# Performance work log

Measured on AMD Instinct MI355X. Metric: run time of the kernel, lower is better.

The kernel has to match this reference:

```python
import jax, jax.numpy as jnp
import numpy as np

N = 100000
E = 6400000
H = 64  # hidden_nf


def setup_inputs() -> dict:
    key = jax.random.key(0)
    ks = jax.random.split(key, 12)
    x = jax.random.normal(ks[0], (N, 3), dtype=jnp.float32)
    vel = jax.random.normal(ks[1], (N, 3), dtype=jnp.float32)
    vel_norm = jax.random.uniform(ks[2], (N, 1), dtype=jnp.float32)
    edge_index = jax.random.randint(ks[3], (2, E), 0, N, dtype=jnp.int32)
    # coord_mlp_vel: Linear(1,H) -> LeakyReLU(0.2) -> Linear(H,1)
    W1 = jax.random.normal(ks[4], (H, 1), dtype=jnp.float32) * (1.0 / np.sqrt(1))
    b1 = jnp.zeros((H,), dtype=jnp.float32)
    W2 = jax.random.normal(ks[5], (1, H), dtype=jnp.float32) * (1.0 / np.sqrt(H))
    b2 = jnp.zeros((1,), dtype=jnp.float32)
    # phi: Linear(1,H) -> LeakyReLU(0.2) -> Linear(H,1,bias=False, xavier gain=0.001) -> Tanh
    Wp1 = jax.random.normal(ks[6], (H, 1), dtype=jnp.float32) * (1.0 / np.sqrt(1))
    bp1 = jnp.zeros((H,), dtype=jnp.float32)
    Wp2 = jax.random.normal(ks[7], (1, H), dtype=jnp.float32) * 0.001
    return {"x": x, "vel_norm": vel_norm, "vel": vel, "edge_index": edge_index,
            "W1": W1, "b1": b1, "W2": W2, "b2": b2,
            "Wp1": Wp1, "bp1": bp1, "Wp2": Wp2}


def reference(x, vel_norm, vel, edge_index, W1, b1, W2, b2, Wp1, bp1, Wp2):
    row, col = edge_index[0], edge_index[1]
    # edge_model: gather endpoint positions, radial distance -> tiny MLP -> scaled diff
    x_diff = x[row] - x[col]                                   # [E, 3]
    radial = jnp.sqrt(jnp.sum(x_diff * x_diff, axis=1, keepdims=True))  # [E, 1]
    h = jax.nn.leaky_relu(radial @ Wp1.T + bp1, 0.2)           # [E, H]
    e_out = jnp.tanh(h @ Wp2.T)                                # [E, 1]
    m_ij = x_diff * e_out                                      # [E, 3]
    # node_model: unsorted_segment_mean over row
    agg_sum = jax.ops.segment_sum(m_ij, row, num_segments=x.shape[0])           # [N, 3]
    cnt = jax.ops.segment_sum(jnp.ones((m_ij.shape[0], 1), m_ij.dtype), row,
                              num_segments=x.shape[0])                           # [N, 1]
    x_out = x + agg_sum / jnp.maximum(cnt, 1.0)
    # velocity term: x + vel * coord_mlp_vel(vel_norm)
    hv = jax.nn.leaky_relu(vel_norm @ W1.T + b1, 0.2)          # [N, H]
    scale = hv @ W2.T + b2                                     # [N, 1]
    return x_out + vel * scale
```

## Files before the change

kernel.cpp:

```cpp
#include <hip/hip_runtime.h>
#include <hip/hip_fp16.h>
#include <math.h>

#define LEAKY 0.2f
#define HDIM 64
#define EPB 2048
#define TPB1 256
#define PERT (EPB / TPB1)
#define RANGE 1024
#define RSH 10
#define KMAX 128
#define NSUB 4
#define NSLICE 8
#define FS2 262144.0f
#define INVFS2 (1.0f / 262144.0f)
#define FBIAS 4194304


__device__ __forceinline__ float fast_tanh(float v) {
    float e = __builtin_amdgcn_exp2f(v * 2.88539008178f);
    return 1.0f - 2.0f * __builtin_amdgcn_rcpf(e + 1.0f);
}

__device__ __forceinline__ float edge_eo(float rad, float C, bool slow,
                                         const float* sW1, const float* sb1,
                                         const float* sW2) {
    if (!slow) return fast_tanh(C * rad);
    float a = 0.f;
    #pragma unroll
    for (int k = 0; k < HDIM; k++) {
        float h = fmaf(rad, sW1[k], sb1[k]);
        h = (h > 0.f) ? h : LEAKY * h;
        a = fmaf(sW2[k], h, a);
    }
    return fast_tanh(a);
}

__global__ void repack_h_kernel(const float* __restrict__ x, uint2* __restrict__ xh, int N,
                                const float* __restrict__ Wp1, const float* __restrict__ bp1,
                                const float* __restrict__ Wp2, float* __restrict__ consts,
                                uint4* __restrict__ acc4, unsigned* __restrict__ cursor, int K) {
    int i = blockIdx.x * blockDim.x + threadIdx.x;
    if (i < N) {
        unsigned hx = __half_as_ushort(__float2half(x[3*i]));
        unsigned hy = __half_as_ushort(__float2half(x[3*i+1]));
        unsigned hz = __half_as_ushort(__float2half(x[3*i+2]));
        xh[i] = make_uint2((hy << 16) | hx, hz);
        acc4[i] = make_uint4(0u, 0u, 0u, 0u);
    }
    if (blockIdx.x == 0) {
        if (threadIdx.x < 64) {
            int k = threadIdx.x;
            float w1 = Wp1[k];
            float slope = (w1 >= 0.f) ? 1.f : LEAKY;
            float c = Wp2[k] * w1 * slope;
            float bnz = (bp1[k] != 0.f) ? 1.f : 0.f;
            #pragma unroll
            for (int off = 32; off > 0; off >>= 1) {
                c += __shfl_down(c, off, 64);
                bnz += __shfl_down(bnz, off, 64);
            }
            if (k == 0) { consts[0] = c; consts[1] = bnz; }
        }
        for (int k = threadIdx.x; k < NSUB * K; k += 256) cursor[k] = 0u;
    }
}

__device__ __forceinline__ unsigned long long pack_rec(float dx, float dy, float dz,
                                                       float eo, unsigned lid) {
    unsigned hx = __half_as_ushort(__float2half(dx * eo));
    unsigned hy = __half_as_ushort(__float2half(dy * eo));
    unsigned hz = __half_as_ushort(__float2half(dz * eo));
    return (unsigned long long)lid
         | ((unsigned long long)hx << 11)
         | ((unsigned long long)hy << 27)
         | ((unsigned long long)hz << 43);
}

__device__ __forceinline__ uint2 make_record(uint2 ga, uint2 gb, int r,
                                             float C, bool slow,
                                             const float* sW1, const float* sb1,
                                             const float* sW2) {
    float ax = __half2float(__ushort_as_half((unsigned short)(ga.x & 0xFFFF)));
    float ay = __half2float(__ushort_as_half((unsigned short)(ga.x >> 16)));
    float az = __half2float(__ushort_as_half((unsigned short)(ga.y & 0xFFFF)));
    float bx = __half2float(__ushort_as_half((unsigned short)(gb.x & 0xFFFF)));
    float by = __half2float(__ushort_as_half((unsigned short)(gb.x >> 16)));
    float bz = __half2float(__ushort_as_half((unsigned short)(gb.y & 0xFFFF)));
    float dx = ax - bx, dy = ay - by, dz = az - bz;
    float rad = sqrtf(dx*dx + dy*dy + dz*dz);
    float eo = edge_eo(rad, C, slow, sW1, sb1, sW2);
    unsigned long long u = pack_rec(dx, dy, dz, eo, (unsigned)r & (RANGE - 1));
    return make_uint2((unsigned)u, (unsigned)(u >> 32));
}

__device__ __forceinline__ void rec_to_acc4(uint2 r, unsigned b_, unsigned* acc4) {
    unsigned long long u = ((unsigned long long)r.y << 32) | r.x;
    unsigned lid = (unsigned)(u & (RANGE - 1));
    unsigned node = b_ * RANGE + lid;
    float mx = __half2float(__ushort_as_half((unsigned short)((u >> 11) & 0xFFFF)));
    float my = __half2float(__ushort_as_half((unsigned short)((u >> 27) & 0xFFFF)));
    float mz = __half2float(__ushort_as_half((unsigned short)((u >> 43) & 0xFFFF)));
    atomicAdd(&acc4[4*node + 0], (unsigned)__float2int_rn(mx * FS2));
    atomicAdd(&acc4[4*node + 1], (unsigned)__float2int_rn(my * FS2));
    atomicAdd(&acc4[4*node + 2], (unsigned)__float2int_rn(mz * FS2));
    atomicAdd(&acc4[4*node + 3], 1u);
}

__global__ __launch_bounds__(TPB1) void fused4_kernel(
        const uint2* __restrict__ xh,
        const int* __restrict__ ei,
        const float* __restrict__ Wp1, const float* __restrict__ bp1,
        const float* __restrict__ Wp2, const float* __restrict__ consts,
        unsigned* __restrict__ cursor, unsigned* __restrict__ acc4,
        uint2* __restrict__ recs, int E, int K, unsigned csub) {
    __shared__ uint2 stage[EPB];
    __shared__ unsigned char bucket_of[EPB];
    __shared__ unsigned hist[KMAX];
    __shared__ unsigned scanv[KMAX + 1];
    __shared__ unsigned gstart[KMAX];
    __shared__ float sW1[HDIM], sb1[HDIM], sW2[HDIM];
    const float C = consts[0];
    const bool slow = (consts[1] != 0.f);
    const unsigned sub = (unsigned)blockIdx.x & (NSUB - 1);
    if (slow) {
        for (int k = threadIdx.x; k < HDIM; k += TPB1) {
            sW1[k] = Wp1[k]; sb1[k] = bp1[k]; sW2[k] = Wp2[k];
        }
    }
    for (int k = threadIdx.x; k < K; k += TPB1) hist[k] = 0;
    __syncthreads();

    const size_t base = (size_t)blockIdx.x * EPB;
    const unsigned t = threadIdx.x;
    uint2 rc[PERT];
    unsigned bk[PERT];
    if (base + EPB <= (size_t)E && (E & 3) == 0) {
        const int4* pr = (const int4*)(ei + base);
        const int4* pc = (const int4*)(ei + (size_t)E + base);
        int4 rv0 = pr[t];
        int4 rv1 = pr[t + TPB1];
        int4 cv0 = pc[t];
        int4 cv1 = pc[t + TPB1];
        uint2 ga0 = xh[rv0.x], ga1 = xh[rv0.y], ga2 = xh[rv0.z], ga3 = xh[rv0.w];
        uint2 ga4 = xh[rv1.x], ga5 = xh[rv1.y], ga6 = xh[rv1.z], ga7 = xh[rv1.w];
        uint2 gb0 = xh[cv0.x], gb1 = xh[cv0.y], gb2 = xh[cv0.z], gb3 = xh[cv0.w];
        uint2 gb4 = xh[cv1.x], gb5 = xh[cv1.y], gb6 = xh[cv1.z], gb7 = xh[cv1.w];
        rc[0] = make_record(ga0, gb0, rv0.x, C, slow, sW1, sb1, sW2);
        rc[1] = make_record(ga1, gb1, rv0.y, C, slow, sW1, sb1, sW2);
        rc[2] = make_record(ga2, gb2, rv0.z, C, slow, sW1, sb1, sW2);
        rc[3] = make_record(ga3, gb3, rv0.w, C, slow, sW1, sb1, sW2);
        rc[4] = make_record(ga4, gb4, rv1.x, C, slow, sW1, sb1, sW2);
        rc[5] = make_record(ga5, gb5, rv1.y, C, slow, sW1, sb1, sW2);
        rc[6] = make_record(ga6, gb6, rv1.z, C, slow, sW1, sb1, sW2);
        rc[7] = make_record(ga7, gb7, rv1.w, C, slow, sW1, sb1, sW2);
        bk[0] = (unsigned)rv0.x >> RSH; bk[1] = (unsigned)rv0.y >> RSH;
        bk[2] = (unsigned)rv0.z >> RSH; bk[3] = (unsigned)rv0.w >> RSH;
        bk[4] = (unsigned)rv1.x >> RSH; bk[5] = (unsigned)rv1.y >> RSH;
        bk[6] = (unsigned)rv1.z >> RSH; bk[7] = (unsigned)rv1.w >> RSH;
        #pragma unroll
        for (int i = 0; i < PERT; i++) atomicAdd(&hist[bk[i]], 1u);
    } else {
        #pragma unroll
        for (int i = 0; i < PERT; i++) {
            size_t e = base + (size_t)i * TPB1 + t;
            bk[i] = 0xFFFFFFFFu;
            if (e < (size_t)E) {
                int r = ei[e];
                int c = ei[(size_t)E + e];
                uint2 ga = xh[r], gb = xh[c];
                rc[i] = make_record(ga, gb, r, C, slow, sW1, sb1, sW2);
                bk[i] = (unsigned)r >> RSH;
                atomicAdd(&hist[bk[i]], 1u);
            }
        }
    }
    __syncthreads();
    unsigned res = 0, myc = 0;
    if (t < (unsigned)K) {
        myc = hist[t];
        if (myc) res = atomicAdd(&cursor[t * NSUB + sub], myc);
    }
    if (t >= 192) {
        int l = t - 192;
        unsigned origA = (l < K) ? hist[l] : 0u;
        unsigned origB = (l + 64 < K) ? hist[l + 64] : 0u;
        unsigned a = origA, b = origB;
        #pragma unroll
        for (int off = 1; off < 64; off <<= 1) {
            unsigned va = __shfl_up(a, off, 64);
            unsigned vb = __shfl_up(b, off, 64);
            if (l >= off) { a += va; b += vb; }
        }
        unsigned totA = __shfl(a, 63, 64);
        unsigned grand = totA + __shfl(b, 63, 64);
        scanv[l] = a - origA;
        scanv[l + 64] = totA + b - origB;
        if (l == 63) scanv[K] = grand;
    }
    __syncthreads();
    if (t < (unsigned)K) gstart[t] = res;
    for (int k = t; k < K; k += TPB1) hist[k] = scanv[k];
    __syncthreads();
    #pragma unroll
    for (int i = 0; i < PERT; i++) {
        if (bk[i] != 0xFFFFFFFFu) {
            unsigned slot = atomicAdd(&hist[bk[i]], 1u);
            stage[slot] = rc[i];
            bucket_of[slot] = (unsigned char)bk[i];
        }
    }
    __syncthreads();
    unsigned total = scanv[K];
    for (unsigned j = t; j < total; j += TPB1) {
        unsigned b_ = bucket_of[j];
        unsigned off = gstart[b_] + (j - scanv[b_]);
        if (off < csub) recs[(size_t)(b_ * NSUB + sub) * csub + off] = stage[j];
        else            rec_to_acc4(stage[j], b_, acc4);
    }
}

__device__ __forceinline__ void proc_rec2(uint2 rv,
                                          unsigned long long* accA,
                                          unsigned long long* accB) {
    unsigned long long u = ((unsigned long long)rv.y << 32) | rv.x;
    unsigned lid = (unsigned)(u & (RANGE - 1));
    float mx = __half2float(__ushort_as_half((unsigned short)((u >> 11) & 0xFFFF)));
    float my = __half2float(__ushort_as_half((unsigned short)((u >> 27) & 0xFFFF)));
    float mz = __half2float(__ushort_as_half((unsigned short)((u >> 43) & 0xFFFF)));
    unsigned ix = (unsigned)(__float2int_rn(mx * FS2) + FBIAS);
    unsigned iy = (unsigned)(__float2int_rn(my * FS2) + FBIAS);
    unsigned iz = (unsigned)(__float2int_rn(mz * FS2) + FBIAS);
    atomicAdd(&accA[lid], ((unsigned long long)ix << 32) | (unsigned long long)iy);
    atomicAdd(&accB[lid], ((unsigned long long)iz << 32) | 1ull);
}

__global__ __launch_bounds__(256) void reduce4_kernel(
        const uint2* __restrict__ recs, const unsigned* __restrict__ cursor,
        uint4* __restrict__ slices, int N, int K, unsigned csub) {
    __shared__ unsigned long long accA[RANGE];
    __shared__ unsigned long long accB[RANGE];
    const int b = blockIdx.x / NSLICE;
    const int s = blockIdx.x % NSLICE;
    const int r = s & (NSUB - 1);
    const int p = s / NSUB;
    for (int i = threadIdx.x; i < RANGE; i += 256) { accA[i] = 0ull; accB[i] = 0ull; }
    __syncthreads();
    unsigned cnt = cursor[b * NSUB + r];
    if (cnt > csub) cnt = csub;
    unsigned per = (cnt + 1) >> 1;
    unsigned st = (unsigned)p * per;
    unsigned en = st + per; if (en > cnt) en = cnt;
    const uint2* rb = recs + (size_t)(b * NSUB + r) * csub;
    unsigned j = st + threadIdx.x;
    if (st < cnt) {
        while (j + 256 < en) {
            uint2 r0 = rb[j];
            uint2 r1 = rb[j + 256];
            proc_rec2(r0, accA, accB);
            proc_rec2(r1, accA, accB);
            j += 512;
        }
        while (j < en) { proc_rec2(rb[j], accA, accB); j += 256; }
    }
    __syncthreads();
    const int nbase = b * RANGE;
    for (int i = threadIdx.x; i < RANGE; i += 256) {
        int node = nbase + i;
        if (node < N) {
            unsigned long long A = accA[i], B = accB[i];
            slices[(size_t)s * N + node] =
                make_uint4((unsigned)(A >> 32), (unsigned)A,
                           (unsigned)(B >> 32), (unsigned)B);
        }
    }
}

__global__ void node_merge_kernel(const float* __restrict__ x,
                                  const float* __restrict__ vel_norm,
                                  const float* __restrict__ vel,
                                  const float* __restrict__ W1, const float* __restrict__ b1,
                                  const float* __restrict__ W2, const float* __restrict__ b2,
                                  const uint4* __restrict__ slices,
                                  const uint4* __restrict__ acc4,
                                  float* __restrict__ out, int N) {
    __shared__ float sW1[HDIM], sb1[HDIM], sW2[HDIM];
    for (int k = threadIdx.x; k < HDIM; k += blockDim.x) {
        sW1[k] = W1[k]; sb1[k] = b1[k]; sW2[k] = W2[k];
    }
    __syncthreads();
    int i = blockIdx.x * blockDim.x + threadIdx.x;
    if (i >= N) return;
    unsigned long long sxb = 0, syb = 0, szb = 0;
    unsigned sc = 0;
    #pragma unroll
    for (int s = 0; s < NSLICE; s++) {
        uint4 v = slices[(size_t)s * N + i];
        sxb += v.x; syb += v.y; szb += v.z; sc += v.w;
    }
    uint4 a4 = acc4[i];
    long long fx = (long long)sxb - (long long)sc * (long long)FBIAS + (long long)(int)a4.x;
    long long fy = (long long)syb - (long long)sc * (long long)FBIAS + (long long)(int)a4.y;
    long long fz = (long long)szb - (long long)sc * (long long)FBIAS + (long long)(int)a4.z;
    float cntf = (float)(sc + a4.w);
    float sx = (float)fx * INVFS2;
    float sy = (float)fy * INVFS2;
    float sz = (float)fz * INVFS2;
    float vn = vel_norm[i];
    float a = b2[0];
    #pragma unroll
    for (int k = 0; k < HDIM; k++) {
        float h = fmaf(vn, sW1[k], sb1[k]);
        h = (h > 0.f) ? h : LEAKY * h;
        a = fmaf(sW2[k], h, a);
    }
    float inv = 1.0f / fmaxf(cntf, 1.0f);
    out[3*i]     = x[3*i]     + sx * inv + vel[3*i]     * a;
    out[3*i + 1] = x[3*i + 1] + sy * inv + vel[3*i + 1] * a;
    out[3*i + 2] = x[3*i + 2] + sz * inv + vel[3*i + 2] * a;
}

__global__ void precompute_kernel(const float* __restrict__ Wp1,
                                  const float* __restrict__ bp1,
                                  const float* __restrict__ Wp2,
                                  float* __restrict__ consts) {
    int k = threadIdx.x;
    float w1 = Wp1[k];
    float slope = (w1 >= 0.f) ? 1.f : LEAKY;
    float c = Wp2[k] * w1 * slope;
    float bnz = (bp1[k] != 0.f) ? 1.f : 0.f;
    #pragma unroll
    for (int off = 32; off > 0; off >>= 1) {
        c += __shfl_down(c, off, 64);
        bnz += __shfl_down(bnz, off, 64);
    }
    if (k == 0) { consts[0] = c; consts[1] = bnz; }
}

__global__ void edge_atomic_kernel(const float* __restrict__ x, const int* __restrict__ ei,
                                   const float* __restrict__ Wp1, const float* __restrict__ bp1,
                                   const float* __restrict__ Wp2, const float* __restrict__ consts,
                                   float* __restrict__ acc, int E) {
    __shared__ float sW1[HDIM], sb1[HDIM], sW2[HDIM];
    const float C = consts[0];
    const bool slow = (consts[1] != 0.f);
    if (slow) {
        for (int k = threadIdx.x; k < HDIM; k += blockDim.x) {
            sW1[k] = Wp1[k]; sb1[k] = bp1[k]; sW2[k] = Wp2[k];
        }
        __syncthreads();
    }
    int e = blockIdx.x * blockDim.x + threadIdx.x;
    if (e >= E) return;
    int r = ei[e];
    int c = ei[E + e];
    float dx = x[3*r] - x[3*c];
    float dy = x[3*r+1] - x[3*c+1];
    float dz = x[3*r+2] - x[3*c+2];
    float rad = sqrtf(dx*dx + dy*dy + dz*dz);
    float eo = edge_eo(rad, C, slow, sW1, sb1, sW2);
    float* basep = acc + ((size_t)r << 2);
    atomicAdd(basep + 0, dx * eo);
    atomicAdd(basep + 1, dy * eo);
    atomicAdd(basep + 2, dz * eo);
    atomicAdd(basep + 3, 1.f);
}

__global__ void node_kernel(const float* __restrict__ x, const float* __restrict__ vel_norm,
                            const float* __restrict__ vel,
                            const float* __restrict__ W1, const float* __restrict__ b1,
                            const float* __restrict__ W2, const float* __restrict__ b2,
                            const float4* __restrict__ slices,
                            float* __restrict__ out, int N, int S) {
    __shared__ float sW1[HDIM], sb1[HDIM], sW2[HDIM];
    for (int k = threadIdx.x; k < HDIM; k += blockDim.x) {
        sW1[k] = W1[k]; sb1[k] = b1[k]; sW2[k] = W2[k];
    }
    __syncthreads();
    int i = blockIdx.x * blockDim.x + threadIdx.x;
    if (i >= N) return;
    float sx = 0.f, sy = 0.f, sz = 0.f, sc = 0.f;
    for (int s = 0; s < S; s++) {
        float4 v = slices[(size_t)s * N + i];
        sx += v.x; sy += v.y; sz += v.z; sc += v.w;
    }
    float vn = vel_norm[i];
    float a = b2[0];
    #pragma unroll
    for (int k = 0; k < HDIM; k++) {
        float h = fmaf(vn, sW1[k], sb1[k]);
        h = (h > 0.f) ? h : LEAKY * h;
        a = fmaf(sW2[k], h, a);
    }
    float inv = 1.0f / fmaxf(sc, 1.0f);
    out[3*i]     = x[3*i]     + sx * inv + vel[3*i]     * a;
    out[3*i + 1] = x[3*i + 1] + sy * inv + vel[3*i + 1] * a;
    out[3*i + 2] = x[3*i + 2] + sz * inv + vel[3*i + 2] * a;
}

extern "C" void kernel_launch(void* const* d_in, const int* in_sizes, int n_in,
                              void* d_out, int out_size, void* d_ws, size_t ws_size,
                              hipStream_t stream) {
    const float* x        = (const float*)d_in[0];
    const float* vel_norm = (const float*)d_in[1];
    const float* vel      = (const float*)d_in[2];
    const int*   ei       = (const int*)  d_in[3];
    const float* W1       = (const float*)d_in[4];
    const float* b1       = (const float*)d_in[5];
    const float* W2       = (const float*)d_in[6];
    const float* b2       = (const float*)d_in[7];
    const float* Wp1      = (const float*)d_in[8];
    const float* bp1      = (const float*)d_in[9];
    const float* Wp2      = (const float*)d_in[10];

    const int N = in_sizes[0] / 3;
    const int E = in_sizes[3] / 2;
    const int K = (N + RANGE - 1) / RANGE;
    const int nblk = (E + EPB - 1) / EPB;

    unsigned csub = (unsigned)(E / (K * NSUB)) + 1024u;
    csub = (csub + 63u) & ~63u;

    size_t rec_bytes = (size_t)K * NSUB * csub * sizeof(uint2);
    size_t sp_slices = rec_bytes;
    size_t sp_xh     = sp_slices + (size_t)NSLICE * N * sizeof(uint4);
    size_t sp_acc    = (sp_xh + (size_t)N * sizeof(uint2) + 15) & ~(size_t)15;
    size_t sp_cur    = sp_acc + (size_t)N * sizeof(uint4);
    size_t sp_const  = (sp_cur + (size_t)NSUB * KMAX * sizeof(unsigned) + 15) & ~(size_t)15;
    size_t need      = sp_const + 32;

    if (K <= KMAX && ws_size >= need) {
        uint2*    recs   = (uint2*)   d_ws;
        uint4*    slices = (uint4*)   ((char*)d_ws + sp_slices);
        uint2*    xh     = (uint2*)   ((char*)d_ws + sp_xh);
        unsigned* acc4   = (unsigned*)((char*)d_ws + sp_acc);
        unsigned* cursor = (unsigned*)((char*)d_ws + sp_cur);
        float*    consts = (float*)   ((char*)d_ws + sp_const);

        repack_h_kernel<<<(N + 255) / 256, 256, 0, stream>>>(
            x, xh, N, Wp1, bp1, Wp2, consts, (uint4*)acc4, cursor, K);
        fused4_kernel<<<nblk, TPB1, 0, stream>>>(
            xh, ei, Wp1, bp1, Wp2, consts, cursor, acc4, recs, E, K, csub);
        reduce4_kernel<<<K * NSLICE, 256, 0, stream>>>(recs, cursor, slices, N, K, csub);
        node_merge_kernel<<<(N + 255) / 256, 256, 0, stream>>>(
            x, vel_norm, vel, W1, b1, W2, b2, slices, (const uint4*)acc4,
            (float*)d_out, N);
    } else {
        float* acc    = (float*)d_ws;
        float* consts = (float*)((char*)d_ws + (size_t)N * sizeof(float4));
        hipMemsetAsync(d_ws, 0, (size_t)N * sizeof(float4) + 32, stream);
        precompute_kernel<<<1, 64, 0, stream>>>(Wp1, bp1, Wp2, consts);
        edge_atomic_kernel<<<(E + 255) / 256, 256, 0, stream>>>(x, ei, Wp1, bp1, Wp2,
                                                                consts, acc, E);
        node_kernel<<<(N + 255) / 256, 256, 0, stream>>>(x, vel_norm, vel, W1, b1, W2, b2,
                                                         (const float4*)acc, (float*)d_out, N, 1);
    }
}
```

Before: 189.4 us.

## Double edges per block, drop a barrier in bucketing, vectorize reduce loads

Each block of the fused edge kernel now handles 4096 edges instead of 2048, so each thread issues twice as many independent gathers and the block count and per-block cursor atomics are halved. The scatter phase uses a separate shared cursor array written during the scan, which removes one __syncthreads and the copy from scanv back into hist. The reduce kernel reads records as 16-byte uint4 pairs and guards the odd tail record. The costs are higher register pressure from 16 records per thread, about twice the shared memory per block, and so possibly lower occupancy.

```diff
diff --git a/kernel.cpp b/kernel.cpp
--- a/kernel.cpp
+++ b/kernel.cpp
@@ -4,7 +4,7 @@
 
 #define LEAKY 0.2f
 #define HDIM 64
-#define EPB 2048
+#define EPB 4096
 #define TPB1 256
 #define PERT (EPB / TPB1)
 #define RANGE 1024
@@ -107,7 +107,7 @@
     atomicAdd(&acc4[4*node + 3], 1u);
 }
 
-__global__ __launch_bounds__(TPB1) void fused4_kernel(
+__global__ __launch_bounds__(TPB1) void fused5_kernel(
         const uint2* __restrict__ xh,
         const int* __restrict__ ei,
         const float* __restrict__ Wp1, const float* __restrict__ bp1,
@@ -118,6 +118,7 @@
     __shared__ unsigned char bucket_of[EPB];
     __shared__ unsigned hist[KMAX];
     __shared__ unsigned scanv[KMAX + 1];
+    __shared__ unsigned cur[KMAX];
     __shared__ unsigned gstart[KMAX];
     __shared__ float sW1[HDIM], sb1[HDIM], sW2[HDIM];
     const float C = consts[0];
@@ -140,24 +141,48 @@
         const int4* pc = (const int4*)(ei + (size_t)E + base);
         int4 rv0 = pr[t];
         int4 rv1 = pr[t + TPB1];
+        int4 rv2 = pr[t + 2 * TPB1];
+        int4 rv3 = pr[t + 3 * TPB1];
         int4 cv0 = pc[t];
         int4 cv1 = pc[t + TPB1];
-        uint2 ga0 = xh[rv0.x], ga1 = xh[rv0.y], ga2 = xh[rv0.z], ga3 = xh[rv0.w];
-        uint2 ga4 = xh[rv1.x], ga5 = xh[rv1.y], ga6 = xh[rv1.z], ga7 = xh[rv1.w];
-        uint2 gb0 = xh[cv0.x], gb1 = xh[cv0.y], gb2 = xh[cv0.z], gb3 = xh[cv0.w];
-        uint2 gb4 = xh[cv1.x], gb5 = xh[cv1.y], gb6 = xh[cv1.z], gb7 = xh[cv1.w];
-        rc[0] = make_record(ga0, gb0, rv0.x, C, slow, sW1, sb1, sW2);
-        rc[1] = make_record(ga1, gb1, rv0.y, C, slow, sW1, sb1, sW2);
-        rc[2] = make_record(ga2, gb2, rv0.z, C, slow, sW1, sb1, sW2);
-        rc[3] = make_record(ga3, gb3, rv0.w, C, slow, sW1, sb1, sW2);
-        rc[4] = make_record(ga4, gb4, rv1.x, C, slow, sW1, sb1, sW2);
-        rc[5] = make_record(ga5, gb5, rv1.y, C, slow, sW1, sb1, sW2);
-        rc[6] = make_record(ga6, gb6, rv1.z, C, slow, sW1, sb1, sW2);
-        rc[7] = make_record(ga7, gb7, rv1.w, C, slow, sW1, sb1, sW2);
-        bk[0] = (unsigned)rv0.x >> RSH; bk[1] = (unsigned)rv0.y >> RSH;
-        bk[2] = (unsigned)rv0.z >> RSH; bk[3] = (unsigned)rv0.w >> RSH;
-        bk[4] = (unsigned)rv1.x >> RSH; bk[5] = (unsigned)rv1.y >> RSH;
-        bk[6] = (unsigned)rv1.z >> RSH; bk[7] = (unsigned)rv1.w >> RSH;
+        int4 cv2 = pc[t + 2 * TPB1];
+        int4 cv3 = pc[t + 3 * TPB1];
+        {
+            uint2 ga0 = xh[rv0.x], ga1 = xh[rv0.y], ga2 = xh[rv0.z], ga3 = xh[rv0.w];
+            uint2 ga4 = xh[rv1.x], ga5 = xh[rv1.y], ga6 = xh[rv1.z], ga7 = xh[rv1.w];
+            uint2 gb0 = xh[cv0.x], gb1 = xh[cv0.y], gb2 = xh[cv0.z], gb3 = xh[cv0.w];
+            uint2 gb4 = xh[cv1.x], gb5 = xh[cv1.y], gb6 = xh[cv1.z], gb7 = xh[cv1.w];
+            rc[0] = make_record(ga0, gb0, rv0.x, C, slow, sW1, sb1, sW2);
+            rc[1] = make_record(ga1, gb1, rv0.y, C, slow, sW1, sb1, sW2);
+            rc[2] = make_record(ga2, gb2, rv0.z, C, slow, sW1, sb1, sW2);
+            rc[3] = make_record(ga3, gb3, rv0.w, C, slow, sW1, sb1, sW2);
+            rc[4] = make_record(ga4, gb4, rv1.x, C, slow, sW1, sb1, sW2);
+            rc[5] = make_record(ga5, gb5, rv1.y, C, slow, sW1, sb1, sW2);
+            rc[6] = make_record(ga6, gb6, rv1.z, C, slow, sW1, sb1, sW2);
+            rc[7] = make_record(ga7, gb7, rv1.w, C, slow, sW1, sb1, sW2);
+        }
+        {
+            uint2 ga0 = xh[rv2.x], ga1 = xh[rv2.y], ga2 = xh[rv2.z], ga3 = xh[rv2.w];
+            uint2 ga4 = xh[rv3.x], ga5 = xh[rv3.y], ga6 = xh[rv3.z], ga7 = xh[rv3.w];
+            uint2 gb0 = xh[cv2.x], gb1 = xh[cv2.y], gb2 = xh[cv2.z], gb3 = xh[cv2.w];
+            uint2 gb4 = xh[cv3.x], gb5 = xh[cv3.y], gb6 = xh[cv3.z], gb7 = xh[cv3.w];
+            rc[8]  = make_record(ga0, gb0, rv2.x, C, slow, sW1, sb1, sW2);
+            rc[9]  = make_record(ga1, gb1, rv2.y, C, slow, sW1, sb1, sW2);
+            rc[10] = make_record(ga2, gb2, rv2.z, C, slow, sW1, sb1, sW2);
+            rc[11] = make_record(ga3, gb3, rv2.w, C, slow, sW1, sb1, sW2);
+            rc[12] = make_record(ga4, gb4, rv3.x, C, slow, sW1, sb1, sW2);
+            rc[13] = make_record(ga5, gb5, rv3.y, C, slow, sW1, sb1, sW2);
+            rc[14] = make_record(ga6, gb6, rv3.z, C, slow, sW1, sb1, sW2);
+            rc[15] = make_record(ga7, gb7, rv3.w, C, slow, sW1, sb1, sW2);
+        }
+        bk[0]  = (unsigned)rv0.x >> RSH; bk[1]  = (unsigned)rv0.y >> RSH;
+        bk[2]  = (unsigned)rv0.z >> RSH; bk[3]  = (unsigned)rv0.w >> RSH;
+        bk[4]  = (unsigned)rv1.x >> RSH; bk[5]  = (unsigned)rv1.y >> RSH;
+        bk[6]  = (unsigned)rv1.z >> RSH; bk[7]  = (unsigned)rv1.w >> RSH;
+        bk[8]  = (unsigned)rv2.x >> RSH; bk[9]  = (unsigned)rv2.y >> RSH;
+        bk[10] = (unsigned)rv2.z >> RSH; bk[11] = (unsigned)rv2.w >> RSH;
+        bk[12] = (unsigned)rv3.x >> RSH; bk[13] = (unsigned)rv3.y >> RSH;
+        bk[14] = (unsigned)rv3.z >> RSH; bk[15] = (unsigned)rv3.w >> RSH;
         #pragma unroll
         for (int i = 0; i < PERT; i++) atomicAdd(&hist[bk[i]], 1u);
     } else {
@@ -176,9 +201,9 @@
         }
     }
     __syncthreads();
-    unsigned res = 0, myc = 0;
+    unsigned res = 0;
     if (t < (unsigned)K) {
-        myc = hist[t];
+        unsigned myc = hist[t];
         if (myc) res = atomicAdd(&cursor[t * NSUB + sub], myc);
     }
     if (t >= 192) {
@@ -194,22 +219,22 @@
         }
         unsigned totA = __shfl(a, 63, 64);
         unsigned grand = totA + __shfl(b, 63, 64);
-        scanv[l] = a - origA;
-        scanv[l + 64] = totA + b - origB;
+        unsigned exA = a - origA;
+        unsigned exB = totA + b - origB;
+        scanv[l] = exA;  cur[l] = exA;
+        scanv[l + 64] = exB;  cur[l + 64] = exB;
         if (l == 63) scanv[K] = grand;
     }
-    __syncthreads();
-    if (t < (unsigned)K) gstart[t] = res;
-    for (int k = t; k < K; k += TPB1) hist[k] = scanv[k];
     __syncthreads();
     #pragma unroll
     for (int i = 0; i < PERT; i++) {
         if (bk[i] != 0xFFFFFFFFu) {
-            unsigned slot = atomicAdd(&hist[bk[i]], 1u);
+            unsigned slot = atomicAdd(&cur[bk[i]], 1u);
             stage[slot] = rc[i];
             bucket_of[slot] = (unsigned char)bk[i];
         }
     }
+    if (t < (unsigned)K) gstart[t] = res;
     __syncthreads();
     unsigned total = scanv[K];
     for (unsigned j = t; j < total; j += TPB1) {
@@ -220,10 +245,10 @@
     }
 }
 
-__device__ __forceinline__ void proc_rec2(uint2 rv,
+__device__ __forceinline__ void proc_rec2(unsigned lo, unsigned hi,
                                           unsigned long long* accA,
                                           unsigned long long* accB) {
-    unsigned long long u = ((unsigned long long)rv.y << 32) | rv.x;
+    unsigned long long u = ((unsigned long long)hi << 32) | lo;
     unsigned lid = (unsigned)(u & (RANGE - 1));
     float mx = __half2float(__ushort_as_half((unsigned short)((u >> 11) & 0xFFFF)));
     float my = __half2float(__ushort_as_half((unsigned short)((u >> 27) & 0xFFFF)));
@@ -235,7 +260,7 @@
     atomicAdd(&accB[lid], ((unsigned long long)iz << 32) | 1ull);
 }
 
-__global__ __launch_bounds__(256) void reduce4_kernel(
+__global__ __launch_bounds__(256) void reduce5_kernel(
         const uint2* __restrict__ recs, const unsigned* __restrict__ cursor,
         uint4* __restrict__ slices, int N, int K, unsigned csub) {
     __shared__ unsigned long long accA[RANGE];
@@ -248,20 +273,28 @@
     __syncthreads();
     unsigned cnt = cursor[b * NSUB + r];
     if (cnt > csub) cnt = csub;
-    unsigned per = (cnt + 1) >> 1;
-    unsigned st = (unsigned)p * per;
-    unsigned en = st + per; if (en > cnt) en = cnt;
-    const uint2* rb = recs + (size_t)(b * NSUB + r) * csub;
-    unsigned j = st + threadIdx.x;
-    if (st < cnt) {
-        while (j + 256 < en) {
-            uint2 r0 = rb[j];
-            uint2 r1 = rb[j + 256];
-            proc_rec2(r0, accA, accB);
-            proc_rec2(r1, accA, accB);
+    unsigned pairs = (cnt + 1) >> 1;
+    unsigned perp = (pairs + 1) >> 1;
+    unsigned p0 = (unsigned)p * perp;
+    unsigned p1 = p0 + perp; if (p1 > pairs) p1 = pairs;
+    const uint4* rb4 = (const uint4*)(recs + (size_t)(b * NSUB + r) * csub);
+    unsigned j = p0 + threadIdx.x;
+    if (p0 < p1) {
+        while (j + 256 < p1) {
+            uint4 v0 = rb4[j];
+            uint4 v1 = rb4[j + 256];
+            proc_rec2(v0.x, v0.y, accA, accB);
+            if (2*j + 1 < cnt) proc_rec2(v0.z, v0.w, accA, accB);
+            proc_rec2(v1.x, v1.y, accA, accB);
+            if (2*(j+256) + 1 < cnt) proc_rec2(v1.z, v1.w, accA, accB);
             j += 512;
         }
-        while (j < en) { proc_rec2(rb[j], accA, accB); j += 256; }
+        while (j < p1) {
+            uint4 v = rb4[j];
+            proc_rec2(v.x, v.y, accA, accB);
+            if (2*j + 1 < cnt) proc_rec2(v.z, v.w, accA, accB);
+            j += 256;
+        }
     }
     __syncthreads();
     const int nbase = b * RANGE;
@@ -439,9 +472,9 @@
 
         repack_h_kernel<<<(N + 255) / 256, 256, 0, stream>>>(
             x, xh, N, Wp1, bp1, Wp2, consts, (uint4*)acc4, cursor, K);
-        fused4_kernel<<<nblk, TPB1, 0, stream>>>(
+        fused5_kernel<<<nblk, TPB1, 0, stream>>>(
             xh, ei, Wp1, bp1, Wp2, consts, cursor, acc4, recs, E, K, csub);
-        reduce4_kernel<<<K * NSLICE, 256, 0, stream>>>(recs, cursor, slices, N, K, csub);
+        reduce5_kernel<<<K * NSLICE, 256, 0, stream>>>(recs, cursor, slices, N, K, csub);
         node_merge_kernel<<<(N + 255) / 256, 256, 0, stream>>>(
             x, vel_norm, vel, W1, b1, W2, b2, slices, (const uint4*)acc4,
             (float*)d_out, N);
```

New measurement: 185.8 us. About the same (-1.9%).

## Bucket raw edge indices in sort pass and compute edge messages during reduction

Applied to the files above, without the earlier changes.

The sort kernel now bins compact 32-bit records (local row id plus column index) instead of computing edge messages and writing 64-bit half-precision records. The x gathers, radial distance and MLP evaluation move into the reduce kernel, where the row endpoint lies in a 1024-node window and is likely cache-resident. This halves record traffic and removes a round of fp16 quantisation of the message, at the cost of random column gathers in the reduce pass. EPB is also doubled to 4096 edges per block.

```diff
diff --git a/kernel.cpp b/kernel.cpp
--- a/kernel.cpp
+++ b/kernel.cpp
@@ -4,7 +4,7 @@
 
 #define LEAKY 0.2f
 #define HDIM 64
-#define EPB 2048
+#define EPB 4096
 #define TPB1 256
 #define PERT (EPB / TPB1)
 #define RANGE 1024
@@ -66,21 +66,13 @@
     }
 }
 
-__device__ __forceinline__ unsigned long long pack_rec(float dx, float dy, float dz,
-                                                       float eo, unsigned lid) {
-    unsigned hx = __half_as_ushort(__float2half(dx * eo));
-    unsigned hy = __half_as_ushort(__float2half(dy * eo));
-    unsigned hz = __half_as_ushort(__float2half(dz * eo));
-    return (unsigned long long)lid
-         | ((unsigned long long)hx << 11)
-         | ((unsigned long long)hy << 27)
-         | ((unsigned long long)hz << 43);
-}
-
-__device__ __forceinline__ uint2 make_record(uint2 ga, uint2 gb, int r,
-                                             float C, bool slow,
-                                             const float* sW1, const float* sb1,
-                                             const float* sW2) {
+__device__ void overflow_edge(unsigned rec, unsigned b_, const uint2* __restrict__ xh,
+                              float C, bool slow,
+                              const float* __restrict__ Wp1, const float* __restrict__ bp1,
+                              const float* __restrict__ Wp2, unsigned* __restrict__ acc4) {
+    unsigned lid = rec >> 17, col = rec & 0x1FFFFu;
+    unsigned row = b_ * RANGE + lid;
+    uint2 ga = xh[row], gb = xh[col];
     float ax = __half2float(__ushort_as_half((unsigned short)(ga.x & 0xFFFF)));
     float ay = __half2float(__ushort_as_half((unsigned short)(ga.x >> 16)));
     float az = __half2float(__ushort_as_half((unsigned short)(ga.y & 0xFFFF)));
@@ -89,75 +81,63 @@
     float bz = __half2float(__ushort_as_half((unsigned short)(gb.y & 0xFFFF)));
     float dx = ax - bx, dy = ay - by, dz = az - bz;
     float rad = sqrtf(dx*dx + dy*dy + dz*dz);
-    float eo = edge_eo(rad, C, slow, sW1, sb1, sW2);
-    unsigned long long u = pack_rec(dx, dy, dz, eo, (unsigned)r & (RANGE - 1));
-    return make_uint2((unsigned)u, (unsigned)(u >> 32));
-}
-
-__device__ __forceinline__ void rec_to_acc4(uint2 r, unsigned b_, unsigned* acc4) {
-    unsigned long long u = ((unsigned long long)r.y << 32) | r.x;
-    unsigned lid = (unsigned)(u & (RANGE - 1));
-    unsigned node = b_ * RANGE + lid;
-    float mx = __half2float(__ushort_as_half((unsigned short)((u >> 11) & 0xFFFF)));
-    float my = __half2float(__ushort_as_half((unsigned short)((u >> 27) & 0xFFFF)));
-    float mz = __half2float(__ushort_as_half((unsigned short)((u >> 43) & 0xFFFF)));
-    atomicAdd(&acc4[4*node + 0], (unsigned)__float2int_rn(mx * FS2));
-    atomicAdd(&acc4[4*node + 1], (unsigned)__float2int_rn(my * FS2));
-    atomicAdd(&acc4[4*node + 2], (unsigned)__float2int_rn(mz * FS2));
-    atomicAdd(&acc4[4*node + 3], 1u);
-}
-
-__global__ __launch_bounds__(TPB1) void fused4_kernel(
+    float eo;
+    if (!slow) {
+        eo = fast_tanh(C * rad);
+    } else {
+        float a = 0.f;
+        for (int k = 0; k < HDIM; k++) {
+            float h = fmaf(rad, Wp1[k], bp1[k]);
+            h = (h > 0.f) ? h : LEAKY * h;
+            a = fmaf(Wp2[k], h, a);
+        }
+        eo = fast_tanh(a);
+    }
+    atomicAdd(&acc4[4*row + 0], (unsigned)__float2int_rn(dx * eo * FS2));
+    atomicAdd(&acc4[4*row + 1], (unsigned)__float2int_rn(dy * eo * FS2));
+    atomicAdd(&acc4[4*row + 2], (unsigned)__float2int_rn(dz * eo * FS2));
+    atomicAdd(&acc4[4*row + 3], 1u);
+}
+
+__global__ __launch_bounds__(TPB1) void sort4_kernel(
+        const int* __restrict__ ei,
         const uint2* __restrict__ xh,
-        const int* __restrict__ ei,
         const float* __restrict__ Wp1, const float* __restrict__ bp1,
         const float* __restrict__ Wp2, const float* __restrict__ consts,
         unsigned* __restrict__ cursor, unsigned* __restrict__ acc4,
-        uint2* __restrict__ recs, int E, int K, unsigned csub) {
-    __shared__ uint2 stage[EPB];
+        unsigned* __restrict__ recs, int E, int K, unsigned csub) {
+    __shared__ unsigned stage[EPB];
     __shared__ unsigned char bucket_of[EPB];
     __shared__ unsigned hist[KMAX];
     __shared__ unsigned scanv[KMAX + 1];
+    __shared__ unsigned cur[KMAX];
     __shared__ unsigned gstart[KMAX];
-    __shared__ float sW1[HDIM], sb1[HDIM], sW2[HDIM];
     const float C = consts[0];
     const bool slow = (consts[1] != 0.f);
     const unsigned sub = (unsigned)blockIdx.x & (NSUB - 1);
-    if (slow) {
-        for (int k = threadIdx.x; k < HDIM; k += TPB1) {
-            sW1[k] = Wp1[k]; sb1[k] = bp1[k]; sW2[k] = Wp2[k];
-        }
-    }
     for (int k = threadIdx.x; k < K; k += TPB1) hist[k] = 0;
     __syncthreads();
 
     const size_t base = (size_t)blockIdx.x * EPB;
     const unsigned t = threadIdx.x;
-    uint2 rc[PERT];
+    unsigned rc[PERT];
     unsigned bk[PERT];
     if (base + EPB <= (size_t)E && (E & 3) == 0) {
         const int4* pr = (const int4*)(ei + base);
         const int4* pc = (const int4*)(ei + (size_t)E + base);
-        int4 rv0 = pr[t];
-        int4 rv1 = pr[t + TPB1];
-        int4 cv0 = pc[t];
-        int4 cv1 = pc[t + TPB1];
-        uint2 ga0 = xh[rv0.x], ga1 = xh[rv0.y], ga2 = xh[rv0.z], ga3 = xh[rv0.w];
-        uint2 ga4 = xh[rv1.x], ga5 = xh[rv1.y], ga6 = xh[rv1.z], ga7 = xh[rv1.w];
-        uint2 gb0 = xh[cv0.x], gb1 = xh[cv0.y], gb2 = xh[cv0.z], gb3 = xh[cv0.w];
-        uint2 gb4 = xh[cv1.x], gb5 = xh[cv1.y], gb6 = xh[cv1.z], gb7 = xh[cv1.w];
-        rc[0] = make_record(ga0, gb0, rv0.x, C, slow, sW1, sb1, sW2);
-        rc[1] = make_record(ga1, gb1, rv0.y, C, slow, sW1, sb1, sW2);
-        rc[2] = make_record(ga2, gb2, rv0.z, C, slow, sW1, sb1, sW2);
-        rc[3] = make_record(ga3, gb3, rv0.w, C, slow, sW1, sb1, sW2);
-        rc[4] = make_record(ga4, gb4, rv1.x, C, slow, sW1, sb1, sW2);
-        rc[5] = make_record(ga5, gb5, rv1.y, C, slow, sW1, sb1, sW2);
-        rc[6] = make_record(ga6, gb6, rv1.z, C, slow, sW1, sb1, sW2);
-        rc[7] = make_record(ga7, gb7, rv1.w, C, slow, sW1, sb1, sW2);
-        bk[0] = (unsigned)rv0.x >> RSH; bk[1] = (unsigned)rv0.y >> RSH;
-        bk[2] = (unsigned)rv0.z >> RSH; bk[3] = (unsigned)rv0.w >> RSH;
-        bk[4] = (unsigned)rv1.x >> RSH; bk[5] = (unsigned)rv1.y >> RSH;
-        bk[6] = (unsigned)rv1.z >> RSH; bk[7] = (unsigned)rv1.w >> RSH;
+        #pragma unroll
+        for (int q = 0; q < PERT / 4; q++) {
+            int4 rv = pr[t + q * TPB1];
+            int4 cv = pc[t + q * TPB1];
+            rc[4*q+0] = (((unsigned)rv.x & (RANGE-1)) << 17) | (unsigned)cv.x;
+            rc[4*q+1] = (((unsigned)rv.y & (RANGE-1)) << 17) | (unsigned)cv.y;
+            rc[4*q+2] = (((unsigned)rv.z & (RANGE-1)) << 17) | (unsigned)cv.z;
+            rc[4*q+3] = (((unsigned)rv.w & (RANGE-1)) << 17) | (unsigned)cv.w;
+            bk[4*q+0] = (unsigned)rv.x >> RSH;
+            bk[4*q+1] = (unsigned)rv.y >> RSH;
+            bk[4*q+2] = (unsigned)rv.z >> RSH;
+            bk[4*q+3] = (unsigned)rv.w >> RSH;
+        }
         #pragma unroll
         for (int i = 0; i < PERT; i++) atomicAdd(&hist[bk[i]], 1u);
     } else {
@@ -166,19 +146,18 @@
             size_t e = base + (size_t)i * TPB1 + t;
             bk[i] = 0xFFFFFFFFu;
             if (e < (size_t)E) {
-                int r = ei[e];
-                int c = ei[(size_t)E + e];
-                uint2 ga = xh[r], gb = xh[c];
-                rc[i] = make_record(ga, gb, r, C, slow, sW1, sb1, sW2);
-                bk[i] = (unsigned)r >> RSH;
+                unsigned r = (unsigned)ei[e];
+                unsigned c = (unsigned)ei[(size_t)E + e];
+                rc[i] = ((r & (RANGE-1)) << 17) | c;
+                bk[i] = r >> RSH;
                 atomicAdd(&hist[bk[i]], 1u);
             }
         }
     }
     __syncthreads();
-    unsigned res = 0, myc = 0;
+    unsigned res = 0;
     if (t < (unsigned)K) {
-        myc = hist[t];
+        unsigned myc = hist[t];
         if (myc) res = atomicAdd(&cursor[t * NSUB + sub], myc);
     }
     if (t >= 192) {
@@ -194,77 +173,91 @@
         }
         unsigned totA = __shfl(a, 63, 64);
         unsigned grand = totA + __shfl(b, 63, 64);
-        scanv[l] = a - origA;
-        scanv[l + 64] = totA + b - origB;
+        unsigned exA = a - origA;
+        unsigned exB = totA + b - origB;
+        scanv[l] = exA;  cur[l] = exA;
+        scanv[l + 64] = exB;  cur[l + 64] = exB;
         if (l == 63) scanv[K] = grand;
     }
-    __syncthreads();
-    if (t < (unsigned)K) gstart[t] = res;
-    for (int k = t; k < K; k += TPB1) hist[k] = scanv[k];
     __syncthreads();
     #pragma unroll
     for (int i = 0; i < PERT; i++) {
         if (bk[i] != 0xFFFFFFFFu) {
-            unsigned slot = atomicAdd(&hist[bk[i]], 1u);
+            unsigned slot = atomicAdd(&cur[bk[i]], 1u);
             stage[slot] = rc[i];
             bucket_of[slot] = (unsigned char)bk[i];
         }
     }
+    if (t < (unsigned)K) gstart[t] = res;
     __syncthreads();
     unsigned total = scanv[K];
     for (unsigned j = t; j < total; j += TPB1) {
         unsigned b_ = bucket_of[j];
         unsigned off = gstart[b_] + (j - scanv[b_]);
         if (off < csub) recs[(size_t)(b_ * NSUB + sub) * csub + off] = stage[j];
-        else            rec_to_acc4(stage[j], b_, acc4);
-    }
-}
-
-__device__ __forceinline__ void proc_rec2(uint2 rv,
-                                          unsigned long long* accA,
-                                          unsigned long long* accB) {
-    unsigned long long u = ((unsigned long long)rv.y << 32) | rv.x;
-    unsigned lid = (unsigned)(u & (RANGE - 1));
-    float mx = __half2float(__ushort_as_half((unsigned short)((u >> 11) & 0xFFFF)));
-    float my = __half2float(__ushort_as_half((unsigned short)((u >> 27) & 0xFFFF)));
-    float mz = __half2float(__ushort_as_half((unsigned short)((u >> 43) & 0xFFFF)));
-    unsigned ix = (unsigned)(__float2int_rn(mx * FS2) + FBIAS);
-    unsigned iy = (unsigned)(__float2int_rn(my * FS2) + FBIAS);
-    unsigned iz = (unsigned)(__float2int_rn(mz * FS2) + FBIAS);
-    atomicAdd(&accA[lid], ((unsigned long long)ix << 32) | (unsigned long long)iy);
-    atomicAdd(&accB[lid], ((unsigned long long)iz << 32) | 1ull);
-}
-
-__global__ __launch_bounds__(256) void reduce4_kernel(
-        const uint2* __restrict__ recs, const unsigned* __restrict__ cursor,
+        else            overflow_edge(stage[j], b_, xh, C, slow, Wp1, bp1, Wp2, acc4);
+    }
+}
+
+__global__ __launch_bounds__(256) void reduce6_kernel(
+        const unsigned* __restrict__ recs, const unsigned* __restrict__ cursor,
+        const uint2* __restrict__ xh,
+        const float* __restrict__ Wp1, const float* __restrict__ bp1,
+        const float* __restrict__ Wp2, const float* __restrict__ consts,
         uint4* __restrict__ slices, int N, int K, unsigned csub) {
     __shared__ unsigned long long accA[RANGE];
     __shared__ unsigned long long accB[RANGE];
+    __shared__ float sW1[HDIM], sb1[HDIM], sW2[HDIM];
     const int b = blockIdx.x / NSLICE;
     const int s = blockIdx.x % NSLICE;
     const int r = s & (NSUB - 1);
     const int p = s / NSUB;
+    const float C = consts[0];
+    const bool slow = (consts[1] != 0.f);
+    if (slow) {
+        for (int k = threadIdx.x; k < HDIM; k += 256) {
+            sW1[k] = Wp1[k]; sb1[k] = bp1[k]; sW2[k] = Wp2[k];
+        }
+    }
     for (int i = threadIdx.x; i < RANGE; i += 256) { accA[i] = 0ull; accB[i] = 0ull; }
     __syncthreads();
+    const int nbase = b * RANGE;
     unsigned cnt = cursor[b * NSUB + r];
     if (cnt > csub) cnt = csub;
-    unsigned per = (cnt + 1) >> 1;
-    unsigned st = (unsigned)p * per;
-    unsigned en = st + per; if (en > cnt) en = cnt;
-    const uint2* rb = recs + (size_t)(b * NSUB + r) * csub;
-    unsigned j = st + threadIdx.x;
-    if (st < cnt) {
-        while (j + 256 < en) {
-            uint2 r0 = rb[j];
-            uint2 r1 = rb[j + 256];
-            proc_rec2(r0, accA, accB);
-            proc_rec2(r1, accA, accB);
-            j += 512;
-        }
-        while (j < en) { proc_rec2(rb[j], accA, accB); j += 256; }
-    }
-    __syncthreads();
-    const int nbase = b * RANGE;
+    unsigned quads = (cnt + 3) >> 2;
+    unsigned perq = (quads + 1) >> 1;
+    unsigned q0 = (unsigned)p * perq;
+    unsigned q1 = q0 + perq; if (q1 > quads) q1 = quads;
+    const uint4* rb4 = (const uint4*)(recs + (size_t)(b * NSUB + r) * csub);
+    for (unsigned q = q0 + threadIdx.x; q < q1; q += 256) {
+        uint4 v = rb4[q];
+        unsigned idx = 4 * q;
+        unsigned rv[4] = {v.x, v.y, v.z, v.w};
+        #pragma unroll
+        for (int u = 0; u < 4; u++) {
+            if (idx + u < cnt) {
+                unsigned rec = rv[u];
+                unsigned lid = rec >> 17, col = rec & 0x1FFFFu;
+                uint2 ga = xh[nbase + lid];
+                uint2 gb = xh[col];
+                float ax = __half2float(__ushort_as_half((unsigned short)(ga.x & 0xFFFF)));
+                float ay = __half2float(__ushort_as_half((unsigned short)(ga.x >> 16)));
+                float az = __half2float(__ushort_as_half((unsigned short)(ga.y & 0xFFFF)));
+                float bx = __half2float(__ushort_as_half((unsigned short)(gb.x & 0xFFFF)));
+                float by = __half2float(__ushort_as_half((unsigned short)(gb.x >> 16)));
+                float bz = __half2float(__ushort_as_half((unsigned short)(gb.y & 0xFFFF)));
+                float dx = ax - bx, dy = ay - by, dz = az - bz;
+                float rad = sqrtf(dx*dx + dy*dy + dz*dz);
+                float eo = edge_eo(rad, C, slow, sW1, sb1, sW2);
+                unsigned ix = (unsigned)(__float2int_rn(dx * eo * FS2) + FBIAS);
+                unsigned iy = (unsigned)(__float2int_rn(dy * eo * FS2) + FBIAS);
+                unsigned iz = (unsigned)(__float2int_rn(dz * eo * FS2) + FBIAS);
+                atomicAdd(&accA[lid], ((unsigned long long)ix << 32) | (unsigned long long)iy);
+                atomicAdd(&accB[lid], ((unsigned long long)iz << 32) | 1ull);
+            }
+        }
+    }
+    __syncthreads();
     for (int i = threadIdx.x; i < RANGE; i += 256) {
         int node = nbase + i;
         if (node < N) {
@@ -421,8 +414,8 @@
     unsigned csub = (unsigned)(E / (K * NSUB)) + 1024u;
     csub = (csub + 63u) & ~63u;
 
-    size_t rec_bytes = (size_t)K * NSUB * csub * sizeof(uint2);
-    size_t sp_slices = rec_bytes;
+    size_t rec_bytes = (size_t)K * NSUB * csub * sizeof(unsigned);
+    size_t sp_slices = (rec_bytes + 15) & ~(size_t)15;
     size_t sp_xh     = sp_slices + (size_t)NSLICE * N * sizeof(uint4);
     size_t sp_acc    = (sp_xh + (size_t)N * sizeof(uint2) + 15) & ~(size_t)15;
     size_t sp_cur    = sp_acc + (size_t)N * sizeof(uint4);
@@ -430,7 +423,7 @@
     size_t need      = sp_const + 32;
 
     if (K <= KMAX && ws_size >= need) {
-        uint2*    recs   = (uint2*)   d_ws;
+        unsigned* recs   = (unsigned*)d_ws;
         uint4*    slices = (uint4*)   ((char*)d_ws + sp_slices);
         uint2*    xh     = (uint2*)   ((char*)d_ws + sp_xh);
         unsigned* acc4   = (unsigned*)((char*)d_ws + sp_acc);
@@ -439,9 +432,10 @@
 
         repack_h_kernel<<<(N + 255) / 256, 256, 0, stream>>>(
             x, xh, N, Wp1, bp1, Wp2, consts, (uint4*)acc4, cursor, K);
-        fused4_kernel<<<nblk, TPB1, 0, stream>>>(
-            xh, ei, Wp1, bp1, Wp2, consts, cursor, acc4, recs, E, K, csub);
-        reduce4_kernel<<<K * NSLICE, 256, 0, stream>>>(recs, cursor, slices, N, K, csub);
+        sort4_kernel<<<nblk, TPB1, 0, stream>>>(
+            ei, xh, Wp1, bp1, Wp2, consts, cursor, acc4, recs, E, K, csub);
+        reduce6_kernel<<<K * NSLICE, 256, 0, stream>>>(
+            recs, cursor, xh, Wp1, bp1, Wp2, consts, slices, N, K, csub);
         node_merge_kernel<<<(N + 255) / 256, 256, 0, stream>>>(
             x, vel_norm, vel, W1, b1, W2, b2, slices, (const uint4*)acc4,
             (float*)d_out, N);
```

Result: slower. 208.2 us (+9.9%).
